# Performance work log

Measured on AMD Instinct MI355X. Metric: run time of the kernel, lower is better.

## Reference

```python
import jax, jax.numpy as jnp
import numpy as np

NUM_HEADS = 16
EPS = 1e-5


def setup_inputs() -> dict:
    key = jax.random.key(0)
    ks = jax.random.split(key, 9)
    B, S, D = 2, 2048, 1024
    s = 1.0 / np.sqrt(D)
    return {
        "x": jax.random.normal(ks[0], (B, S, D), dtype=jnp.float32),
        "Wq": jax.random.uniform(ks[1], (D, D), jnp.float32, -s, s),
        "bq": jax.random.uniform(ks[2], (D,), jnp.float32, -s, s),
        "Wk": jax.random.uniform(ks[3], (D, D), jnp.float32, -s, s),
        "bk": jax.random.uniform(ks[4], (D,), jnp.float32, -s, s),
        "Wv": jax.random.uniform(ks[5], (D, D), jnp.float32, -s, s),
        "bv": jax.random.uniform(ks[6], (D,), jnp.float32, -s, s),
        "Wo": jax.random.uniform(ks[7], (D, D), jnp.float32, -s, s),
        "bo": jax.random.uniform(ks[8], (D,), jnp.float32, -s, s),
    }


def reference(x, Wq, bq, Wk, bk, Wv, bv, Wo, bo):
    B, S, D = x.shape
    H = NUM_HEADS
    hd = D // H
    # projections -> [B, H, S, hd]
    def proj(W, b):
        return (x @ W + b).reshape(B, S, H, hd).transpose(0, 2, 1, 3)
    Q = proj(Wq, bq)
    K = proj(Wk, bk)
    V = proj(Wv, bv)
    scores = jnp.einsum("bhqd,bhkd->bhqk", Q, K) / jnp.sqrt(jnp.float32(hd))
    attn = jax.nn.softmax(scores, axis=-1)  # dropout is identity in eval mode
    out = jnp.einsum("bhqk,bhkd->bhqd", attn, V)
    out = out.transpose(0, 2, 1, 3).reshape(B, S, D)
    out = jax.nn.relu(out @ Wo + bo)
    mu = jnp.mean(out, axis=-1, keepdims=True)
    var = jnp.var(out, axis=-1, keepdims=True)
    return (out - mu) * jax.lax.rsqrt(var + EPS)
```

## Files before the change

kernel.cpp:

```cpp
#include <hip/hip_runtime.h>
#include <hip/hip_bf16.h>
#include <math.h>

#define Bb 2
#define Ss 2048
#define Dd 1024
#define Hh 16
#define HD 64
#define Mm (Bb*Ss)

typedef __attribute__((ext_vector_type(8))) short bf8_t;
typedef __attribute__((ext_vector_type(4))) float f4_t;
typedef __attribute__((ext_vector_type(2))) unsigned u2_t;

#define LOG2E 1.4426950408889634f

#define AS1 __attribute__((address_space(1)))
#define AS3 __attribute__((address_space(3)))

__device__ __forceinline__ void gl2lds16(const void* g, void* l) {
    __builtin_amdgcn_global_load_lds((const AS1 unsigned int*)g,
                                     (AS3 unsigned int*)l, 16, 0, 0);
}
__device__ __forceinline__ short bfr(float f) {
    __hip_bfloat16 h = __float2bfloat16(f);
    return *reinterpret_cast<short*>(&h);
}
__device__ __forceinline__ unsigned pkbf16(float a, float b) {
    const unsigned ua = __builtin_bit_cast(unsigned, a) + 0x8000u;
    const unsigned ub = __builtin_bit_cast(unsigned, b) + 0x8000u;
    return __builtin_amdgcn_perm(ub, ua, 0x07060302u);
}
__device__ __forceinline__ float fexp2(float x) {
    return __builtin_amdgcn_exp2f(x);
}
__device__ __forceinline__ float b2f(unsigned short u) {
    return __builtin_bit_cast(float, (unsigned)u << 16);
}

__global__ __launch_bounds__(256)
void prep(const float* __restrict__ x,
          const float* __restrict__ w0, const float* __restrict__ w1,
          const float* __restrict__ w2, const float* __restrict__ w3,
          __hip_bfloat16* __restrict__ Wt4, __hip_bfloat16* __restrict__ Xh)
{
    const int z = blockIdx.z;
    if (z < 4) {
        const float* W = (z == 0) ? w0 : (z == 1) ? w1 : (z == 2) ? w2 : w3;
        __hip_bfloat16* Wt = Wt4 + (size_t)z * Dd * Dd;
        __shared__ float t[32][33];
        const int n0 = blockIdx.x * 32, k0 = blockIdx.y * 32;
        const int tx = threadIdx.x & 31, ty = threadIdx.x >> 5;
        #pragma unroll
        for (int rr = 0; rr < 4; ++rr)
            t[ty + rr*8][tx] = W[(size_t)(k0 + ty + rr*8) * Dd + n0 + tx];
        __syncthreads();
        #pragma unroll
        for (int rr = 0; rr < 4; ++rr)
            Wt[(size_t)(n0 + ty + rr*8) * Dd + k0 + tx] =
                __float2bfloat16(t[tx][ty + rr*8]);
    } else {
        const int bid = (z - 4) * 1024 + blockIdx.y * 32 + blockIdx.x;
        const size_t i = ((size_t)bid * 256 + threadIdx.x) * 8;
        const float4 a = *(const float4*)&x[i];
        const float4 b = *(const float4*)&x[i + 4];
        bf8_t o;
        o[0] = bfr(a.x); o[1] = bfr(a.y); o[2] = bfr(a.z); o[3] = bfr(a.w);
        o[4] = bfr(b.x); o[5] = bfr(b.y); o[6] = bfr(b.z); o[7] = bfr(b.w);
        *(bf8_t*)&Xh[i] = o;
    }
}

__global__ __launch_bounds__(256)
void gemm_qkv(const __hip_bfloat16* __restrict__ A,
              const __hip_bfloat16* __restrict__ Bt,
              const float* __restrict__ b0, const float* __restrict__ b1,
              const float* __restrict__ b2,
              __hip_bfloat16* __restrict__ Qh, __hip_bfloat16* __restrict__ Kh,
              __hip_bfloat16* __restrict__ Vt)
{
    __shared__ __align__(16) char pool[34816];
    __hip_bfloat16* As = (__hip_bfloat16*)pool;
    __hip_bfloat16* Bs = As + 2 * 128 * 32;

    const int tid  = threadIdx.x;
    const int wave = tid >> 6;
    const int lane = tid & 63;
    const int llo  = lane & 15;
    const int lhi  = lane >> 4;
    const int wm   = wave & 1;
    const int wn   = wave >> 1;
    const int row0 = blockIdx.y * 128;
    const int col0 = blockIdx.x * 128;

    size_t aoff[2], boff[2];
    int    loff[2];
    #pragma unroll
    for (int p = 0; p < 2; ++p) {
        const int g = p * 256 + wave * 64 + lane;
        const int r = g >> 2, kc = (g & 3) * 8;
        aoff[p] = (size_t)(row0 + r) * Dd + kc;
        boff[p] = (size_t)(col0 + r) * Dd + kc;
        loff[p] = (p * 256 + wave * 64) * 16;
    }
    const __hip_bfloat16* Acur = A;
    const __hip_bfloat16* Bcur = Bt;

    auto stage = [&](int buf) {
        #pragma unroll
        for (int p = 0; p < 2; ++p) {
            gl2lds16(Acur + aoff[p], (char*)As + buf*8192 + loff[p]);
            gl2lds16(Bcur + boff[p], (char*)Bs + buf*8192 + loff[p]);
        }
        Acur += 32; Bcur += 32;
    };

    f4_t acc[4][4] = {};
    stage(0);
    for (int kt = 0; kt < 32; ++kt) {
        const int buf = kt & 1;
        __syncthreads();
        if (kt + 1 < 32) stage(buf ^ 1);

        bf8_t a[4], b[4];
        #pragma unroll
        for (int i = 0; i < 4; ++i)
            a[i] = *(const bf8_t*)&As[buf*4096 + (wm*64 + i*16 + llo) * 32 + lhi*8];
        #pragma unroll
        for (int j = 0; j < 4; ++j)
            b[j] = *(const bf8_t*)&Bs[buf*4096 + (wn*64 + j*16 + llo) * 32 + lhi*8];
        #pragma unroll
        for (int i = 0; i < 4; ++i)
            #pragma unroll
            for (int j = 0; j < 4; ++j)
                acc[i][j] = __builtin_amdgcn_mfma_f32_16x16x32_bf16(
                    a[i], b[j], acc[i][j], 0, 0, 0);
    }

    const int sel   = col0 >> 10;
    const int cbase = col0 & 1023;
    __hip_bfloat16* Ls = (__hip_bfloat16*)pool;
    __syncthreads();

    float bv[4];
    const float* bp = (sel == 0) ? b0 : (sel == 1) ? b1 : b2;
    #pragma unroll
    for (int j = 0; j < 4; ++j) bv[j] = bp[cbase + wn*64 + j*16 + llo];
    const float scale = (sel == 0) ? 0.125f * LOG2E : 1.0f;

    if (sel < 2) {
        #pragma unroll
        for (int i = 0; i < 4; ++i)
            #pragma unroll
            for (int r = 0; r < 4; ++r) {
                const int ml = wm*64 + i*16 + lhi*4 + r;
                #pragma unroll
                for (int j = 0; j < 4; ++j)
                    Ls[ml*136 + wn*64 + j*16 + llo] =
                        __float2bfloat16((acc[i][j][r] + bv[j]) * scale);
            }
        __syncthreads();
        __hip_bfloat16* outQK = (sel == 0) ? Qh : Kh;
        #pragma unroll
        for (int p = 0; p < 8; ++p) {
            const int id = p*256 + tid;
            const int rl = id >> 4;
            const int c8 = (id & 15) * 8;
            const bf8_t v = *(const bf8_t*)&Ls[rl*136 + c8];
            const int m  = row0 + rl;
            const int b_ = m >> 11, s_ = m & (Ss - 1);
            const int col = cbase + c8;
            *(bf8_t*)&outQK[((size_t)(b_*Hh + (col >> 6))*Ss + s_)*HD + (col & 63)] = v;
        }
    } else {
        #pragma unroll
        for (int i = 0; i < 4; ++i)
            #pragma unroll
            for (int r = 0; r < 4; ++r) {
                const int ml = wm*64 + i*16 + lhi*4 + r;
                #pragma unroll
                for (int j = 0; j < 4; ++j)
                    Ls[(wn*64 + j*16 + llo)*136 + ml] =
                        __float2bfloat16(acc[i][j][r] + bv[j]);
            }
        __syncthreads();
        const int b_ = row0 >> 11;
        const int sb = row0 & (Ss - 1);
        #pragma unroll
        for (int p = 0; p < 8; ++p) {
            const int cl = p*16 + (tid >> 4);
            const int m  = (tid & 15) * 8;
            const bf8_t v = *(const bf8_t*)&Ls[cl*136 + m];
            const int cc = cbase + cl;
            *(bf8_t*)&Vt[((size_t)(b_*Hh + (cc >> 6))*HD + (cc & 63))*Ss + sb + m] = v;
        }
    }
}

__global__ __launch_bounds__(256, 2)
void attn_mfma(const __hip_bfloat16* __restrict__ Qh,
               const __hip_bfloat16* __restrict__ Kh,
               const __hip_bfloat16* __restrict__ Vt,
               __hip_bfloat16* __restrict__ Ah)
{
    const int b    = blockIdx.z;
    const int h    = blockIdx.y;
    const int wave = threadIdx.x >> 6;
    const int lane = threadIdx.x & 63;
    const int llo  = lane & 15;
    const int lhi  = lane >> 4;
    const int qb   = blockIdx.x * 128 + wave * 32;

    const size_t base = ((size_t)(b*Hh + h)) * Ss * HD;

    __shared__ __hip_bfloat16 Ks[2][2 * 64 * 32];
    __shared__ __hip_bfloat16 Vs[2][2 * 64 * 32];
    __shared__ __hip_bfloat16 Pl[4][32 * 64];
    __hip_bfloat16* Pw = &Pl[wave][0];

    int koff[2], voff[2], loff[2];
    #pragma unroll
    for (int it = 0; it < 2; ++it) {
        const int g  = it*256 + wave*64 + lane;
        const int hf = g >> 8;
        const int rr = (g >> 2) & 63;
        const int c8 = (g & 3) * 8;
        koff[it] = rr*HD + hf*32 + c8;
        voff[it] = rr*Ss + hf*32 + c8;
        loff[it] = (it*256 + wave*64) * 16;
    }
    const __hip_bfloat16* Kcur = Kh + base;
    const __hip_bfloat16* Vcur = Vt + base;

    auto stage = [&](int buf) {
        #pragma unroll
        for (int it = 0; it < 2; ++it) {
            gl2lds16(Kcur + koff[it], (char*)&Ks[buf][0] + loff[it]);
            gl2lds16(Vcur + voff[it], (char*)&Vs[buf][0] + loff[it]);
        }
        Kcur += 64 * HD;
        Vcur += 64;
    };

    bf8_t qf[2][2];
    #pragma unroll
    for (int s = 0; s < 2; ++s)
        #pragma unroll
        for (int d = 0; d < 2; ++d)
            qf[s][d] = *(const bf8_t*)&Qh[base + (size_t)(qb + 16*s + llo)*HD + 32*d + lhi*8];

    f4_t o_[2][4];
    float lacc[2];
    #pragma unroll
    for (int s = 0; s < 2; ++s) {
        #pragma unroll
        for (int n = 0; n < 4; ++n) o_[s][n] = (f4_t){0.f,0.f,0.f,0.f};
        lacc[s] = 0.f;
    }

    const f4_t zf = {0.f,0.f,0.f,0.f};
    const int llo7 = llo & 7;

    stage(0);

    for (int t = 0; t < Ss/64; ++t) {
        const int buf = t & 1;
        __syncthreads();
        if (t + 1 < Ss/64) stage(buf ^ 1);

        bf8_t kf[4][2];
        #pragma unroll
        for (int kc = 0; kc < 4; ++kc)
            #pragma unroll
            for (int d = 0; d < 2; ++d)
                kf[kc][d] = *(const bf8_t*)&Ks[buf][d*2048 + (kc*16 + llo)*32 + lhi*8];

        f4_t sacc[2][4];
        #pragma unroll
        for (int s = 0; s < 2; ++s)
            #pragma unroll
            for (int kc = 0; kc < 4; ++kc) {
                sacc[s][kc] = __builtin_amdgcn_mfma_f32_16x16x32_bf16(kf[kc][0], qf[s][0], zf, 0, 0, 0);
                sacc[s][kc] = __builtin_amdgcn_mfma_f32_16x16x32_bf16(kf[kc][1], qf[s][1], sacc[s][kc], 0, 0, 0);
            }

        #pragma unroll
        for (int s = 0; s < 2; ++s) {
            #pragma unroll
            for (int kc = 0; kc < 4; ++kc) {
                const float p0 = fexp2(sacc[s][kc][0]);
                const float p1 = fexp2(sacc[s][kc][1]);
                const float p2 = fexp2(sacc[s][kc][2]);
                const float p3 = fexp2(sacc[s][kc][3]);
                lacc[s] += (p0 + p1) + (p2 + p3);
                const u2_t pk = { pkbf16(p0, p1), pkbf16(p2, p3) };
                const int phys = (2*kc + (lhi >> 1)) ^ llo7;
                *(u2_t*)&Pw[(16*s + llo)*64 + phys*8 + (lhi & 1)*4] = pk;
            }
        }
        asm volatile("s_waitcnt lgkmcnt(0)" ::: "memory");

        #pragma unroll
        for (int d = 0; d < 2; ++d) {
            bf8_t pf[2];
            #pragma unroll
            for (int s = 0; s < 2; ++s)
                pf[s] = *(const bf8_t*)&Pw[(16*s + llo)*64 + (((4*d + lhi) ^ llo7) << 3)];
            #pragma unroll
            for (int nc = 0; nc < 4; ++nc) {
                const bf8_t vf = *(const bf8_t*)&Vs[buf][d*2048 + (nc*16 + llo)*32 + lhi*8];
                #pragma unroll
                for (int s = 0; s < 2; ++s)
                    o_[s][nc] = __builtin_amdgcn_mfma_f32_16x16x32_bf16(pf[s], vf, o_[s][nc], 0, 0, 0);
            }
        }
    }

    #pragma unroll
    for (int s = 0; s < 2; ++s) {
        lacc[s] += __shfl_xor(lacc[s], 16);
        lacc[s] += __shfl_xor(lacc[s], 32);
    }

    #pragma unroll
    for (int s = 0; s < 2; ++s) {
        #pragma unroll
        for (int r = 0; r < 4; ++r) {
            const float lv  = __shfl(lacc[s], 4*lhi + r);
            const float inv = 1.0f / lv;
            const int q = qb + 16*s + 4*lhi + r;
            __hip_bfloat16* orow = &Ah[((size_t)(b*Ss) + q)*Dd + h*HD + llo];
            #pragma unroll
            for (int nc = 0; nc < 4; ++nc)
                orow[16*nc] = __float2bfloat16(o_[s][nc][r] * inv);
        }
    }
}

__global__ __launch_bounds__(256)
void gemm_out(const __hip_bfloat16* __restrict__ A,
              const __hip_bfloat16* __restrict__ Bt,
              __hip_bfloat16* __restrict__ Ro)
{
    __shared__ __hip_bfloat16 As[2][128 * 32];
    __shared__ __hip_bfloat16 Bs[2][128 * 32];

    const int tid  = threadIdx.x;
    const int wave = tid >> 6;
    const int lane = tid & 63;
    const int llo  = lane & 15;
    const int lhi  = lane >> 4;
    const int wm   = wave & 1;
    const int wn   = wave >> 1;
    const int row0 = blockIdx.y * 128;
    const int col0 = blockIdx.x * 128;
    const int z    = blockIdx.z;

    size_t aoff[2], boff[2];
    int    loff[2];
    #pragma unroll
    for (int p = 0; p < 2; ++p) {
        const int g = p * 256 + wave * 64 + lane;
        const int r = g >> 2, kc = (g & 3) * 8;
        aoff[p] = (size_t)(row0 + r) * Dd + kc;
        boff[p] = (size_t)(col0 + r) * Dd + kc;
        loff[p] = (p * 256 + wave * 64) * 16;
    }
    const __hip_bfloat16* Acur = A  + (size_t)z * (Dd/2);
    const __hip_bfloat16* Bcur = Bt + (size_t)z * (Dd/2);

    auto stage = [&](int buf) {
        #pragma unroll
        for (int p = 0; p < 2; ++p) {
            gl2lds16(Acur + aoff[p], (char*)&As[buf][0] + loff[p]);
            gl2lds16(Bcur + boff[p], (char*)&Bs[buf][0] + loff[p]);
        }
        Acur += 32; Bcur += 32;
    };

    f4_t acc[4][4] = {};
    stage(0);
    for (int kt = 0; kt < 16; ++kt) {
        const int buf = kt & 1;
        __syncthreads();
        if (kt + 1 < 16) stage(buf ^ 1);

        bf8_t a[4], b[4];
        #pragma unroll
        for (int i = 0; i < 4; ++i)
            a[i] = *(const bf8_t*)&As[buf][(wm*64 + i*16 + llo) * 32 + lhi*8];
        #pragma unroll
        for (int j = 0; j < 4; ++j)
            b[j] = *(const bf8_t*)&Bs[buf][(wn*64 + j*16 + llo) * 32 + lhi*8];
        #pragma unroll
        for (int i = 0; i < 4; ++i)
            #pragma unroll
            for (int j = 0; j < 4; ++j)
                acc[i][j] = __builtin_amdgcn_mfma_f32_16x16x32_bf16(
                    a[i], b[j], acc[i][j], 0, 0, 0);
    }

    __hip_bfloat16* Roz = Ro + (size_t)z * Mm * Dd;
    #pragma unroll
    for (int i = 0; i < 4; ++i) {
        #pragma unroll
        for (int r = 0; r < 4; ++r) {
            const int m = row0 + wm*64 + i*16 + lhi*4 + r;
            #pragma unroll
            for (int j = 0; j < 4; ++j) {
                const int col = col0 + wn*64 + j*16 + llo;
                Roz[(size_t)m * Dd + col] = __float2bfloat16(acc[i][j][r]);
            }
        }
    }
}

__global__ __launch_bounds__(256)
void layernorm(const __hip_bfloat16* __restrict__ P0,
               const __hip_bfloat16* __restrict__ P1,
               const float* __restrict__ bias, float* __restrict__ out)
{
    const int row = blockIdx.x;
    const int c = threadIdx.x;
    const ushort4 a = ((const ushort4*)(P0 + (size_t)row*Dd))[c];
    const ushort4 b = ((const ushort4*)(P1 + (size_t)row*Dd))[c];
    const float4 bb = ((const float4*)bias)[c];
    float4 v;
    v.x = fmaxf(b2f(a.x) + b2f(b.x) + bb.x, 0.0f);
    v.y = fmaxf(b2f(a.y) + b2f(b.y) + bb.y, 0.0f);
    v.z = fmaxf(b2f(a.z) + b2f(b.z) + bb.z, 0.0f);
    v.w = fmaxf(b2f(a.w) + b2f(b.w) + bb.w, 0.0f);

    float s  = v.x + v.y + v.z + v.w;
    float ss = v.x*v.x + v.y*v.y + v.z*v.z + v.w*v.w;
    #pragma unroll
    for (int off = 32; off > 0; off >>= 1) {
        s  += __shfl_down(s,  off);
        ss += __shfl_down(ss, off);
    }
    __shared__ float rs[4], rss[4];
    const int wid = c >> 6, lid = c & 63;
    if (lid == 0) { rs[wid] = s; rss[wid] = ss; }
    __syncthreads();
    s  = rs[0] + rs[1] + rs[2] + rs[3];
    ss = rss[0] + rss[1] + rss[2] + rss[3];
    const float mean = s * (1.0f / Dd);
    const float var  = ss * (1.0f / Dd) - mean * mean;
    const float rstd = rsqrtf(var + 1e-5f);
    float4 o;
    o.x = (v.x - mean) * rstd;
    o.y = (v.y - mean) * rstd;
    o.z = (v.z - mean) * rstd;
    o.w = (v.w - mean) * rstd;
    ((float4*)(out + (size_t)row*Dd))[c] = o;
}

extern "C" void kernel_launch(void* const* d_in, const int* in_sizes, int n_in,
                              void* d_out, int out_size, void* d_ws, size_t ws_size,
                              hipStream_t stream)
{
    const float* x  = (const float*)d_in[0];
    const float* Wq = (const float*)d_in[1];
    const float* bq = (const float*)d_in[2];
    const float* Wk = (const float*)d_in[3];
    const float* bk = (const float*)d_in[4];
    const float* Wv = (const float*)d_in[5];
    const float* bv = (const float*)d_in[6];
    const float* Wo = (const float*)d_in[7];
    const float* bo = (const float*)d_in[8];
    float* out = (float*)d_out;

    __hip_bfloat16* Xh    = (__hip_bfloat16*)d_ws;
    __hip_bfloat16* Wqkvt = Xh    + (size_t)Mm*Dd;
    __hip_bfloat16* Wot   = Wqkvt + (size_t)3*Dd*Dd;
    __hip_bfloat16* Ah    = Wot   + (size_t)Dd*Dd;
    __hip_bfloat16* Qh    = Ah    + (size_t)Mm*Dd;
    __hip_bfloat16* Kh    = Qh    + (size_t)Mm*Dd;
    __hip_bfloat16* Vt    = Kh    + (size_t)Mm*Dd;
    __hip_bfloat16* Rb    = Qh;

    prep<<<dim3(32, 32, 6), dim3(256), 0, stream>>>(x, Wq, Wk, Wv, Wo, Wqkvt, Xh);
    gemm_qkv<<<dim3(3*Dd/128, Mm/128), dim3(256), 0, stream>>>(
        Xh, Wqkvt, bq, bk, bv, Qh, Kh, Vt);
    attn_mfma<<<dim3(Ss/128, Hh, Bb), dim3(256), 0, stream>>>(Qh, Kh, Vt, Ah);
    gemm_out<<<dim3(Dd/128, Mm/128, 2), dim3(256), 0, stream>>>(Ah, Wot, Rb);
    layernorm<<<dim3(Mm), dim3(256), 0, stream>>>(Rb, Rb + (size_t)Mm*Dd, bo, out);
}
```

Before: 203.2 us.

## Swizzle LDS tiles and move attention P to registers via permlane swaps

Applies an XOR swizzle to the 16-byte chunk index when staging A/B tiles in both GEMMs and K/V tiles in attention, with matching swizzled reads, to cut LDS bank conflicts on the MFMA operand loads. In the attention kernel, the softmax probabilities are no longer written to and reread from a per-wave LDS buffer. They are rearranged into the MFMA A-operand layout with v_permlane32_swap/v_permlane16_swap. This removes LDS traffic and an lgkmcnt wait per tile, at the cost of more live registers (V fragments are now preloaded), which could reduce occupancy.

```diff
diff --git a/kernel.cpp b/kernel.cpp
--- a/kernel.cpp
+++ b/kernel.cpp
@@ -11,7 +11,8 @@
 
 typedef __attribute__((ext_vector_type(8))) short bf8_t;
 typedef __attribute__((ext_vector_type(4))) float f4_t;
-typedef __attribute__((ext_vector_type(2))) unsigned u2_t;
+typedef __attribute__((ext_vector_type(4))) unsigned u4_t;
+typedef __attribute__((ext_vector_type(2))) unsigned uint2v;
 
 #define LOG2E 1.4426950408889634f
 
@@ -36,6 +37,22 @@
 }
 __device__ __forceinline__ float b2f(unsigned short u) {
     return __builtin_bit_cast(float, (unsigned)u << 16);
+}
+__device__ __forceinline__ void pl32(unsigned &a, unsigned &b) {
+#if __has_builtin(__builtin_amdgcn_permlane32_swap)
+    uint2v r = __builtin_amdgcn_permlane32_swap(a, b, false, false);
+    a = r[0]; b = r[1];
+#else
+    asm volatile("v_permlane32_swap_b32 %0, %1" : "+v"(a), "+v"(b));
+#endif
+}
+__device__ __forceinline__ void pl16(unsigned &a, unsigned &b) {
+#if __has_builtin(__builtin_amdgcn_permlane16_swap)
+    uint2v r = __builtin_amdgcn_permlane16_swap(a, b, false, false);
+    a = r[0]; b = r[1];
+#else
+    asm volatile("v_permlane16_swap_b32 %0, %1" : "+v"(a), "+v"(b));
+#endif
 }
 
 __global__ __launch_bounds__(256)
@@ -98,7 +115,8 @@
     #pragma unroll
     for (int p = 0; p < 2; ++p) {
         const int g = p * 256 + wave * 64 + lane;
-        const int r = g >> 2, kc = (g & 3) * 8;
+        const int r = g >> 2;
+        const int kc = ((g & 3) ^ ((r >> 1) & 3)) * 8;
         aoff[p] = (size_t)(row0 + r) * Dd + kc;
         boff[p] = (size_t)(col0 + r) * Dd + kc;
         loff[p] = (p * 256 + wave * 64) * 16;
@@ -114,6 +132,8 @@
         }
         Acur += 32; Bcur += 32;
     };
+
+    const int xch = (lhi ^ ((llo >> 1) & 3)) * 8;
 
     f4_t acc[4][4] = {};
     stage(0);
@@ -125,10 +145,10 @@
         bf8_t a[4], b[4];
         #pragma unroll
         for (int i = 0; i < 4; ++i)
-            a[i] = *(const bf8_t*)&As[buf*4096 + (wm*64 + i*16 + llo) * 32 + lhi*8];
+            a[i] = *(const bf8_t*)&As[buf*4096 + (wm*64 + i*16 + llo) * 32 + xch];
         #pragma unroll
         for (int j = 0; j < 4; ++j)
-            b[j] = *(const bf8_t*)&Bs[buf*4096 + (wn*64 + j*16 + llo) * 32 + lhi*8];
+            b[j] = *(const bf8_t*)&Bs[buf*4096 + (wn*64 + j*16 + llo) * 32 + xch];
         #pragma unroll
         for (int i = 0; i < 4; ++i)
             #pragma unroll
@@ -215,8 +235,6 @@
 
     __shared__ __hip_bfloat16 Ks[2][2 * 64 * 32];
     __shared__ __hip_bfloat16 Vs[2][2 * 64 * 32];
-    __shared__ __hip_bfloat16 Pl[4][32 * 64];
-    __hip_bfloat16* Pw = &Pl[wave][0];
 
     int koff[2], voff[2], loff[2];
     #pragma unroll
@@ -224,7 +242,7 @@
         const int g  = it*256 + wave*64 + lane;
         const int hf = g >> 8;
         const int rr = (g >> 2) & 63;
-        const int c8 = (g & 3) * 8;
+        const int c8 = ((g & 3) ^ ((rr >> 1) & 3)) * 8;
         koff[it] = rr*HD + hf*32 + c8;
         voff[it] = rr*Ss + hf*32 + c8;
         loff[it] = (it*256 + wave*64) * 16;
@@ -259,7 +277,7 @@
     }
 
     const f4_t zf = {0.f,0.f,0.f,0.f};
-    const int llo7 = llo & 7;
+    const int xch = (lhi ^ ((llo >> 1) & 3)) * 8;
 
     stage(0);
 
@@ -273,7 +291,7 @@
         for (int kc = 0; kc < 4; ++kc)
             #pragma unroll
             for (int d = 0; d < 2; ++d)
-                kf[kc][d] = *(const bf8_t*)&Ks[buf][d*2048 + (kc*16 + llo)*32 + lhi*8];
+                kf[kc][d] = *(const bf8_t*)&Ks[buf][d*2048 + (kc*16 + llo)*32 + xch];
 
         f4_t sacc[2][4];
         #pragma unroll
@@ -284,8 +302,17 @@
                 sacc[s][kc] = __builtin_amdgcn_mfma_f32_16x16x32_bf16(kf[kc][1], qf[s][1], sacc[s][kc], 0, 0, 0);
             }
 
+        bf8_t vf[4][2];
+        #pragma unroll
+        for (int nc = 0; nc < 4; ++nc)
+            #pragma unroll
+            for (int d = 0; d < 2; ++d)
+                vf[nc][d] = *(const bf8_t*)&Vs[buf][d*2048 + (nc*16 + llo)*32 + xch];
+
+        bf8_t pf[2][2];
         #pragma unroll
         for (int s = 0; s < 2; ++s) {
+            unsigned w[4][2];
             #pragma unroll
             for (int kc = 0; kc < 4; ++kc) {
                 const float p0 = fexp2(sacc[s][kc][0]);
@@ -293,27 +320,31 @@
                 const float p2 = fexp2(sacc[s][kc][2]);
                 const float p3 = fexp2(sacc[s][kc][3]);
                 lacc[s] += (p0 + p1) + (p2 + p3);
-                const u2_t pk = { pkbf16(p0, p1), pkbf16(p2, p3) };
-                const int phys = (2*kc + (lhi >> 1)) ^ llo7;
-                *(u2_t*)&Pw[(16*s + llo)*64 + phys*8 + (lhi & 1)*4] = pk;
+                w[kc][0] = pkbf16(p0, p1);
+                w[kc][1] = pkbf16(p2, p3);
             }
-        }
-        asm volatile("s_waitcnt lgkmcnt(0)" ::: "memory");
-
-        #pragma unroll
-        for (int d = 0; d < 2; ++d) {
-            bf8_t pf[2];
-            #pragma unroll
-            for (int s = 0; s < 2; ++s)
-                pf[s] = *(const bf8_t*)&Pw[(16*s + llo)*64 + (((4*d + lhi) ^ llo7) << 3)];
-            #pragma unroll
-            for (int nc = 0; nc < 4; ++nc) {
-                const bf8_t vf = *(const bf8_t*)&Vs[buf][d*2048 + (nc*16 + llo)*32 + lhi*8];
+            #pragma unroll
+            for (int d = 0; d < 2; ++d) {
+                u4_t pu;
+                #pragma unroll
+                for (int hh = 0; hh < 2; ++hh) {
+                    unsigned U = w[2*d][hh], V = w[2*d+1][hh];
+                    pl32(U, V);
+                    pl16(U, V);
+                    pu[hh]     = U;
+                    pu[2 + hh] = V;
+                }
+                pf[s][d] = __builtin_bit_cast(bf8_t, pu);
+            }
+        }
+
+        #pragma unroll
+        for (int d = 0; d < 2; ++d)
+            #pragma unroll
+            for (int nc = 0; nc < 4; ++nc)
                 #pragma unroll
                 for (int s = 0; s < 2; ++s)
-                    o_[s][nc] = __builtin_amdgcn_mfma_f32_16x16x32_bf16(pf[s], vf, o_[s][nc], 0, 0, 0);
-            }
-        }
+                    o_[s][nc] = __builtin_amdgcn_mfma_f32_16x16x32_bf16(pf[s][d], vf[nc][d], o_[s][nc], 0, 0, 0);
     }
 
     #pragma unroll
@@ -361,7 +392,8 @@
     #pragma unroll
     for (int p = 0; p < 2; ++p) {
         const int g = p * 256 + wave * 64 + lane;
-        const int r = g >> 2, kc = (g & 3) * 8;
+        const int r = g >> 2;
+        const int kc = ((g & 3) ^ ((r >> 1) & 3)) * 8;
         aoff[p] = (size_t)(row0 + r) * Dd + kc;
         boff[p] = (size_t)(col0 + r) * Dd + kc;
         loff[p] = (p * 256 + wave * 64) * 16;
@@ -377,6 +409,8 @@
         }
         Acur += 32; Bcur += 32;
     };
+
+    const int xch = (lhi ^ ((llo >> 1) & 3)) * 8;
 
     f4_t acc[4][4] = {};
     stage(0);
@@ -388,10 +422,10 @@
         bf8_t a[4], b[4];
         #pragma unroll
         for (int i = 0; i < 4; ++i)
-            a[i] = *(const bf8_t*)&As[buf][(wm*64 + i*16 + llo) * 32 + lhi*8];
+            a[i] = *(const bf8_t*)&As[buf][(wm*64 + i*16 + llo) * 32 + xch];
         #pragma unroll
         for (int j = 0; j < 4; ++j)
-            b[j] = *(const bf8_t*)&Bs[buf][(wn*64 + j*16 + llo) * 32 + lhi*8];
+            b[j] = *(const bf8_t*)&Bs[buf][(wn*64 + j*16 + llo) * 32 + xch];
         #pragma unroll
         for (int i = 0; i < 4; ++i)
             #pragma unroll
```

Result: faster. 198.6 us (-2.3%).
